# Kernel tuning notes

Hardware: AMD Instinct MI355X
Metric: run time of the kernel (lower is better)

## Reference

```python
import jax, jax.numpy as jnp
import numpy as np

# module hyperparams (from init_kwargs)
C, O, G, E, W, KS = 64, 64, 16, 128, 7, 2
AH, AS = 2, 2              # activate_height, activate_stride
D = C // G                 # kernel depth per group = 4
N = O // G                 # filters per group = 4
EPS = 1e-5                 # BatchNorm eps
LEAKY = 0.01               # LeakyReLU negative slope
B, T = 2, 512


def setup_inputs() -> dict:
    key = jax.random.key(0)
    k1, k2 = jax.random.split(key)
    x = jax.random.normal(k1, (B, C, E, T), dtype=jnp.float32)
    weight = jax.random.normal(k2, (O, D, E, W), dtype=jnp.float32) * 0.05
    gamma = jnp.ones((O,), jnp.float32)
    beta = jnp.zeros((O,), jnp.float32)
    return {"x": x, "weight": weight, "gamma": gamma, "beta": beta}


def reference(x, weight, gamma, beta):
    b, c, f, T_in = x.shape
    pad = W // 2
    xp = jnp.pad(x, ((0, 0), (0, 0), (0, 0), (pad, pad)))
    t = (T_in + 2 * pad - W) // KS + 1
    # unfold: window index grid [t, W]
    idx = KS * jnp.arange(t)[:, None] + jnp.arange(W)[None, :]
    xu = xp[..., idx]                        # [b, c, f, t, W]
    xu = xu.reshape(b, G, D, f, t, W)        # channel = (g d), group-major
    wg = weight.reshape(G, N, D, f, W)       # out = (g n)
    # broadcast elementwise mul -> [b, g, n, d, f, t, w]
    y = xu[:, :, None] * wg[None, :, :, :, :, None, :]
    y = y.reshape(b, O, D, f, t, W)          # (g n) -> o
    # BatchNorm3d over channel O, training-mode batch stats (biased var)
    mean = y.mean(axis=(0, 2, 3, 4, 5), keepdims=True)
    var = y.var(axis=(0, 2, 3, 4, 5), keepdims=True)
    y = (y - mean) * jax.lax.rsqrt(var + EPS)
    bshape = (1, O, 1, 1, 1, 1)
    y = y * gamma.reshape(bshape) + beta.reshape(bshape)
    ys = y.sum(axis=(2, 5))                  # [b, o, f, t]
    yp = jax.lax.reduce_window(ys, jnp.float32(0), jax.lax.add,
                               (1, 1, AH, 1), (1, 1, AS, 1), 'VALID')  # [b,o,fo,t]
    return jnp.where(yp >= 0, yp, LEAKY * yp)
```

## Files before the change

kernel.cpp:

```cpp
#include <hip/hip_runtime.h>

constexpr int Cc = 64, Oc = 64, Gc = 16, Ec = 128, Wc = 7;
constexpr int Dc = 4, Nc = 4, Bc = 2, Tc = 512, TTc = 256, FOc = 64;
constexpr float EPSf = 1e-5f, LEAKYf = 0.01f;
constexpr float Minv = 1.0f / 1835008.0f;


__global__ __launch_bounds__(256) void fused_k(const float* __restrict__ x,
                                               const float* __restrict__ wgt,
                                               float* __restrict__ raw,
                                               float* __restrict__ partials) {
  int bid = blockIdx.x;
  int fo  = bid & 63;
  int g   = (bid >> 6) & 15;
  int b   = bid >> 10;
  int tid = threadIdx.x;

  __shared__ float xs[8 * 520];
  __shared__ float wsm[224];
  __shared__ float rowsum[4][4][2];
  __shared__ float QL[8][7];

  int f2 = tid >> 7;
  int j  = tid & 127;
  float se2p[4], so2p[4];
#pragma unroll
  for (int dd = 0; dd < 4; ++dd) {
    const float4* src = (const float4*)(
        x + ((size_t)((b * Cc + g * Dc + dd) * Ec + 2 * fo + f2)) * Tc);
    float4 v = src[j];
    float* row = &xs[(dd * 2 + f2) * 520];
    int q0 = 4 + 4 * j;
    row[((q0 + 0) & 7) * 65 + ((q0 + 0) >> 3)] = v.x;
    row[((q0 + 1) & 7) * 65 + ((q0 + 1) >> 3)] = v.y;
    row[((q0 + 2) & 7) * 65 + ((q0 + 2) >> 3)] = v.z;
    row[((q0 + 3) & 7) * 65 + ((q0 + 3) >> 3)] = v.w;
    se2p[dd] = v.x * v.x + v.z * v.z;
    so2p[dd] = v.y * v.y + v.w * v.w;
  }
  if (tid < 64) {
    int r = tid >> 3, jj = tid & 7;
    int q = (jj < 4) ? jj : (512 + jj);
    xs[r * 520 + (q & 7) * 65 + (q >> 3)] = 0.f;
  }
  if (tid < 224) {
    int n = tid / 56, rr = tid % 56;
    int dd = rr / 14, r2 = rr % 14;
    int ff = r2 / 7, w = r2 % 7;
    int o = g * Nc + n;
    wsm[tid] = wgt[((size_t)((o * Dc + dd) * Ec + 2 * fo + ff)) * Wc + w];
  }
#pragma unroll
  for (int off = 1; off < 64; off <<= 1) {
#pragma unroll
    for (int dd = 0; dd < 4; ++dd) {
      se2p[dd] += __shfl_xor(se2p[dd], off);
      so2p[dd] += __shfl_xor(so2p[dd], off);
    }
  }
  int lane = tid & 63, wv = tid >> 6;
  if (lane == 0) {
#pragma unroll
    for (int dd = 0; dd < 4; ++dd) {
      rowsum[wv][dd][0] = se2p[dd];
      rowsum[wv][dd][1] = so2p[dd];
    }
  }
  __syncthreads();

  if (tid < 8) {
    int r = tid, ddi = r >> 1, f2i = r & 1;
    const float* row = &xs[r * 520];
    float e0 = row[260], e1 = row[325], e509 = row[129], e510 = row[194],
          e511 = row[259];
    float se2 = rowsum[f2i * 2][ddi][0] + rowsum[f2i * 2 + 1][ddi][0];
    float so2 = rowsum[f2i * 2][ddi][1] + rowsum[f2i * 2 + 1][ddi][1];
    QL[r][0] = so2 - e509 * e509 - e511 * e511;
    QL[r][1] = se2 - e510 * e510;
    QL[r][2] = so2 - e511 * e511;
    QL[r][3] = se2;
    QL[r][4] = so2;
    QL[r][5] = se2 - e0 * e0;
    QL[r][6] = so2 - e1 * e1;
  }
  __syncthreads();

  int n  = tid >> 6;
  int jj = tid & 63;
  float a0 = 0.f, a1 = 0.f, a2 = 0.f, a3 = 0.f;
#pragma unroll
  for (int r = 0; r < 8; ++r) {
    const float* row = &xs[r * 520];
    float xv[13];
#pragma unroll
    for (int i = 0; i < 13; ++i) {
      int c = 1 + i;
      xv[i] = row[(c & 7) * 65 + (c >> 3) + jj];
    }
    const float* wp = &wsm[(n * 8 + r) * 7];
#pragma unroll
    for (int w = 0; w < 7; ++w) {
      float wt = wp[w];
      a0 += xv[w]     * wt;
      a1 += xv[w + 2] * wt;
      a2 += xv[w + 4] * wt;
      a3 += xv[w + 6] * wt;
    }
  }
  int o = g * Nc + n;
  float4 res; res.x = a0; res.y = a1; res.z = a2; res.w = a3;
  *(float4*)(raw + ((size_t)((b * Oc + o) * FOc + fo)) * TTc + 4 * jj) = res;

  float msum = a0 + a1 + a2 + a3;
#pragma unroll
  for (int off = 1; off < 64; off <<= 1) msum += __shfl_xor(msum, off);
  if (jj == 0) partials[bid * 8 + n] = msum;

  if (tid < 4) {
    float vp = 0.f;
#pragma unroll
    for (int r = 0; r < 8; ++r) {
#pragma unroll
      for (int w = 0; w < 7; ++w) {
        float wt = wsm[(tid * 8 + r) * 7 + w];
        vp += QL[r][w] * wt * wt;
      }
    }
    partials[bid * 8 + 4 + tid] = vp;
  }
}

__global__ __launch_bounds__(256) void finish_k(const float* __restrict__ raw,
                                                const float* __restrict__ partials,
                                                const float* __restrict__ gamma,
                                                const float* __restrict__ beta,
                                                float* __restrict__ out) {
  int bid = blockIdx.x;
  int seg = bid & 15;
  int o   = (bid >> 4) & 63;
  int b   = bid >> 10;
  int tid = threadIdx.x;
  int g = o >> 2, n = o & 3;

  __shared__ float red[2][2];
  __shared__ float sAC[2];

  float mp = 0.f, vp = 0.f;
  if (tid < 128) {
    int b2 = tid >> 6, fo = tid & 63;
    const float* p = &partials[(size_t)(((b2 << 4) | g) << 6 | fo) * 8];
    mp = p[n];
    vp = p[4 + n];
  }
#pragma unroll
  for (int off = 1; off < 64; off <<= 1) {
    mp += __shfl_xor(mp, off);
    vp += __shfl_xor(vp, off);
  }
  int lane = tid & 63, wv = tid >> 6;
  if (lane == 0 && wv < 2) { red[wv][0] = mp; red[wv][1] = vp; }
  __syncthreads();
  if (tid == 0) {
    float mean = (red[0][0] + red[1][0]) * Minv;
    float e2   = (red[0][1] + red[1][1]) * Minv;
    float var  = e2 - mean * mean;
    float a    = gamma[o] * rsqrtf(var + EPSf);
    sAC[0] = a;
    sAC[1] = 56.0f * (beta[o] - a * mean);
  }
  __syncthreads();

  float a = sAC[0], c = sAC[1];
  size_t base = ((size_t)(b * Oc + o)) * (FOc * TTc) + seg * 1024 + tid * 4;
  float4 v = *(const float4*)(raw + base);
  float4 res;
  float r0 = a * v.x + c; res.x = (r0 >= 0.f) ? r0 : LEAKYf * r0;
  float r1 = a * v.y + c; res.y = (r1 >= 0.f) ? r1 : LEAKYf * r1;
  float r2 = a * v.z + c; res.z = (r2 >= 0.f) ? r2 : LEAKYf * r2;
  float r3 = a * v.w + c; res.w = (r3 >= 0.f) ? r3 : LEAKYf * r3;
  *(float4*)(out + base) = res;
}

extern "C" void kernel_launch(void* const* d_in, const int* in_sizes, int n_in,
                              void* d_out, int out_size, void* d_ws, size_t ws_size,
                              hipStream_t stream) {
  (void)in_sizes; (void)n_in; (void)out_size; (void)ws_size;
  const float* x     = (const float*)d_in[0];
  const float* w     = (const float*)d_in[1];
  const float* gamma = (const float*)d_in[2];
  const float* beta  = (const float*)d_in[3];
  float* raw      = (float*)d_ws;
  float* partials = raw + (size_t)Bc * Oc * FOc * TTc;
  fused_k<<<dim3(Bc * Gc * FOc), dim3(256), 0, stream>>>(x, w, raw, partials);
  finish_k<<<dim3(Bc * Oc * 16), dim3(256), 0, stream>>>(raw, partials, gamma,
                                                         beta, (float*)d_out);
}
```

Before: 92.87 us.

## Process two output rows per block with float4 shared layout and register tiling

The fused kernel now handles two pooled frequency rows per block, halving the grid. Input rows are staged in shared memory as padded float4 with a swizzled layout so both loads and window reads are vectorised. Each thread computes two output channels times four time steps, reusing the loaded x values across channels. Sum-of-squares statistics are recomputed from shared memory instead of during the load. This doubles shared memory per block and raises register pressure, which may lower occupancy.

Measured after the change: 91.48 us. No clear change (-1.5%).

```diff
diff --git a/kernel.cpp b/kernel.cpp
--- a/kernel.cpp
+++ b/kernel.cpp
@@ -5,128 +5,147 @@
 constexpr float EPSf = 1e-5f, LEAKYf = 0.01f;
 constexpr float Minv = 1.0f / 1835008.0f;
 
+
+__device__ __forceinline__ int FL4(int c) { return (c & 3) * 33 + (c >> 2); }
 
 __global__ __launch_bounds__(256) void fused_k(const float* __restrict__ x,
                                                const float* __restrict__ wgt,
                                                float* __restrict__ raw,
                                                float* __restrict__ partials) {
   int bid = blockIdx.x;
-  int fo  = bid & 63;
-  int g   = (bid >> 6) & 15;
-  int b   = bid >> 10;
-  int tid = threadIdx.x;
-
-  __shared__ float xs[8 * 520];
-  __shared__ float wsm[224];
-  __shared__ float rowsum[4][4][2];
-  __shared__ float QL[8][7];
-
-  int f2 = tid >> 7;
-  int j  = tid & 127;
-  float se2p[4], so2p[4];
-#pragma unroll
-  for (int dd = 0; dd < 4; ++dd) {
+  int fo2 = bid & 31;
+  int g   = (bid >> 5) & 15;
+  int b   = bid >> 9;
+  int t   = threadIdx.x;
+
+  __shared__ float xs[16 * 528];
+  __shared__ float wsm[512];
+  __shared__ float QS[16][2];
+  __shared__ float QL[16][7];
+
+  float4* xs4 = (float4*)xs;
+
+#pragma unroll
+  for (int k = 0; k < 8; ++k) {
+    int idx = t + 256 * k;
+    int lr = idx >> 7, jj = idx & 127;
+    int fo_l = lr >> 3, dd = (lr >> 1) & 3, f2 = lr & 1;
     const float4* src = (const float4*)(
-        x + ((size_t)((b * Cc + g * Dc + dd) * Ec + 2 * fo + f2)) * Tc);
-    float4 v = src[j];
-    float* row = &xs[(dd * 2 + f2) * 520];
-    int q0 = 4 + 4 * j;
-    row[((q0 + 0) & 7) * 65 + ((q0 + 0) >> 3)] = v.x;
-    row[((q0 + 1) & 7) * 65 + ((q0 + 1) >> 3)] = v.y;
-    row[((q0 + 2) & 7) * 65 + ((q0 + 2) >> 3)] = v.z;
-    row[((q0 + 3) & 7) * 65 + ((q0 + 3) >> 3)] = v.w;
-    se2p[dd] = v.x * v.x + v.z * v.z;
-    so2p[dd] = v.y * v.y + v.w * v.w;
-  }
-  if (tid < 64) {
-    int r = tid >> 3, jj = tid & 7;
-    int q = (jj < 4) ? jj : (512 + jj);
-    xs[r * 520 + (q & 7) * 65 + (q >> 3)] = 0.f;
-  }
-  if (tid < 224) {
-    int n = tid / 56, rr = tid % 56;
-    int dd = rr / 14, r2 = rr % 14;
-    int ff = r2 / 7, w = r2 % 7;
-    int o = g * Nc + n;
-    wsm[tid] = wgt[((size_t)((o * Dc + dd) * Ec + 2 * fo + ff)) * Wc + w];
-  }
-#pragma unroll
-  for (int off = 1; off < 64; off <<= 1) {
-#pragma unroll
-    for (int dd = 0; dd < 4; ++dd) {
-      se2p[dd] += __shfl_xor(se2p[dd], off);
-      so2p[dd] += __shfl_xor(so2p[dd], off);
-    }
-  }
-  int lane = tid & 63, wv = tid >> 6;
-  if (lane == 0) {
-#pragma unroll
-    for (int dd = 0; dd < 4; ++dd) {
-      rowsum[wv][dd][0] = se2p[dd];
-      rowsum[wv][dd][1] = so2p[dd];
-    }
-  }
-  __syncthreads();
-
-  if (tid < 8) {
-    int r = tid, ddi = r >> 1, f2i = r & 1;
-    const float* row = &xs[r * 520];
-    float e0 = row[260], e1 = row[325], e509 = row[129], e510 = row[194],
-          e511 = row[259];
-    float se2 = rowsum[f2i * 2][ddi][0] + rowsum[f2i * 2 + 1][ddi][0];
-    float so2 = rowsum[f2i * 2][ddi][1] + rowsum[f2i * 2 + 1][ddi][1];
-    QL[r][0] = so2 - e509 * e509 - e511 * e511;
-    QL[r][1] = se2 - e510 * e510;
-    QL[r][2] = so2 - e511 * e511;
-    QL[r][3] = se2;
-    QL[r][4] = so2;
-    QL[r][5] = se2 - e0 * e0;
-    QL[r][6] = so2 - e1 * e1;
-  }
-  __syncthreads();
-
-  int n  = tid >> 6;
-  int jj = tid & 63;
-  float a0 = 0.f, a1 = 0.f, a2 = 0.f, a3 = 0.f;
-#pragma unroll
-  for (int r = 0; r < 8; ++r) {
-    const float* row = &xs[r * 520];
-    float xv[13];
-#pragma unroll
-    for (int i = 0; i < 13; ++i) {
-      int c = 1 + i;
-      xv[i] = row[(c & 7) * 65 + (c >> 3) + jj];
-    }
-    const float* wp = &wsm[(n * 8 + r) * 7];
+        x + ((size_t)((b * Cc + g * Dc + dd) * Ec + 4 * fo2 + 2 * fo_l + f2)) * Tc);
+    float4 v = src[jj];
+    xs4[lr * 132 + FL4(jj + 1)] = v;
+  }
+  if (t < 32) {
+    int lr = t >> 1;
+    int c = (t & 1) ? 129 : 0;
+    xs4[lr * 132 + FL4(c)] = make_float4(0.f, 0.f, 0.f, 0.f);
+  }
+  if (t < 128) {
+#pragma unroll
+    for (int i = 0; i < 4; ++i) {
+      int s = t * 4 + i;
+      int w = s & 7, n = (s >> 3) & 3, lr8 = (s >> 5) & 7, fo_l = s >> 8;
+      int o = g * Nc + n, dd = lr8 >> 1, f = 4 * fo2 + 2 * fo_l + (lr8 & 1);
+      wsm[s] = (w < 7) ? wgt[((size_t)((o * Dc + dd) * Ec + f)) * Wc + w] : 0.f;
+    }
+  }
+  __syncthreads();
+
+  {
+    int row = t >> 4, sub = t & 15;
+    float se2 = 0.f, so2 = 0.f;
+#pragma unroll
+    for (int k = 0; k < 8; ++k) {
+      int c = 1 + sub + 16 * k;
+      float4 v = xs4[row * 132 + FL4(c)];
+      se2 += v.x * v.x + v.z * v.z;
+      so2 += v.y * v.y + v.w * v.w;
+    }
+#pragma unroll
+    for (int off = 1; off < 16; off <<= 1) {
+      se2 += __shfl_xor(se2, off);
+      so2 += __shfl_xor(so2, off);
+    }
+    if (sub == 0) { QS[row][0] = se2; QS[row][1] = so2; }
+  }
+
+  int wv = t >> 6, j = t & 63;
+  int fo_l = wv >> 1, n0 = (wv & 1) * 2;
+  int fo = fo2 * 2 + fo_l;
+  float acc0[4] = {0.f, 0.f, 0.f, 0.f}, acc1[4] = {0.f, 0.f, 0.f, 0.f};
+#pragma unroll
+  for (int lr8 = 0; lr8 < 8; ++lr8) {
+    const float4* rb = xs4 + (fo_l * 8 + lr8) * 132;
+    float4 X0 = rb[FL4(2 * j)];
+    float4 X1 = rb[FL4(2 * j + 1)];
+    float4 X2 = rb[FL4(2 * j + 2)];
+    float4 X3 = rb[FL4(2 * j + 3)];
+    float xq[16] = {X0.x, X0.y, X0.z, X0.w, X1.x, X1.y, X1.z, X1.w,
+                    X2.x, X2.y, X2.z, X2.w, X3.x, X3.y, X3.z, X3.w};
+    const float4* wb = (const float4*)&wsm[((fo_l * 8 + lr8) * 4 + n0) * 8];
+    float4 Wa0 = wb[0], Wa1 = wb[1], Wb0 = wb[2], Wb1 = wb[3];
+    float wA[7] = {Wa0.x, Wa0.y, Wa0.z, Wa0.w, Wa1.x, Wa1.y, Wa1.z};
+    float wB[7] = {Wb0.x, Wb0.y, Wb0.z, Wb0.w, Wb1.x, Wb1.y, Wb1.z};
 #pragma unroll
     for (int w = 0; w < 7; ++w) {
-      float wt = wp[w];
-      a0 += xv[w]     * wt;
-      a1 += xv[w + 2] * wt;
-      a2 += xv[w + 4] * wt;
-      a3 += xv[w + 6] * wt;
-    }
-  }
-  int o = g * Nc + n;
-  float4 res; res.x = a0; res.y = a1; res.z = a2; res.w = a3;
-  *(float4*)(raw + ((size_t)((b * Oc + o) * FOc + fo)) * TTc + 4 * jj) = res;
-
-  float msum = a0 + a1 + a2 + a3;
-#pragma unroll
-  for (int off = 1; off < 64; off <<= 1) msum += __shfl_xor(msum, off);
-  if (jj == 0) partials[bid * 8 + n] = msum;
-
-  if (tid < 4) {
+#pragma unroll
+      for (int s = 0; s < 4; ++s) {
+        float xv = xq[2 * s + w + 1];
+        acc0[s] += xv * wA[w];
+        acc1[s] += xv * wB[w];
+      }
+    }
+  }
+  {
+    int o0 = g * Nc + n0;
+    float4 r0 = make_float4(acc0[0], acc0[1], acc0[2], acc0[3]);
+    float4 r1 = make_float4(acc1[0], acc1[1], acc1[2], acc1[3]);
+    *(float4*)(raw + ((size_t)((b * Oc + o0) * FOc + fo)) * TTc + 4 * j) = r0;
+    *(float4*)(raw + ((size_t)((b * Oc + o0 + 1) * FOc + fo)) * TTc + 4 * j) = r1;
+  }
+  {
+    float ms0 = acc0[0] + acc0[1] + acc0[2] + acc0[3];
+    float ms1 = acc1[0] + acc1[1] + acc1[2] + acc1[3];
+#pragma unroll
+    for (int off = 1; off < 64; off <<= 1) {
+      ms0 += __shfl_xor(ms0, off);
+      ms1 += __shfl_xor(ms1, off);
+    }
+    if (j == 0) {
+      float* p = &partials[((size_t)((b * Gc + g) * FOc + fo)) * 8];
+      p[n0] = ms0;
+      p[n0 + 1] = ms1;
+    }
+  }
+  __syncthreads();
+
+  if (t < 16) {
+    int row = t;
+    const float* rowf = &xs[row * 528];
+    float e509 = rowf[129], e510 = rowf[130], e511 = rowf[131];
+    float e0 = rowf[132], e1 = rowf[133];
+    float se2 = QS[row][0], so2 = QS[row][1];
+    QL[row][0] = so2 - e509 * e509 - e511 * e511;
+    QL[row][1] = se2 - e510 * e510;
+    QL[row][2] = so2 - e511 * e511;
+    QL[row][3] = se2;
+    QL[row][4] = so2;
+    QL[row][5] = se2 - e0 * e0;
+    QL[row][6] = so2 - e1 * e1;
+  }
+  __syncthreads();
+  if (t < 8) {
+    int fl = t >> 2, n = t & 3;
     float vp = 0.f;
 #pragma unroll
-    for (int r = 0; r < 8; ++r) {
+    for (int lr8 = 0; lr8 < 8; ++lr8) {
 #pragma unroll
       for (int w = 0; w < 7; ++w) {
-        float wt = wsm[(tid * 8 + r) * 7 + w];
-        vp += QL[r][w] * wt * wt;
+        float wt = wsm[((fl * 8 + lr8) * 4 + n) * 8 + w];
+        vp += QL[fl * 8 + lr8][w] * wt * wt;
       }
     }
-    partials[bid * 8 + 4 + tid] = vp;
+    partials[((size_t)((b * Gc + g) * FOc + fo2 * 2 + fl)) * 8 + 4 + n] = vp;
   }
 }
 
@@ -191,7 +210,7 @@
   const float* beta  = (const float*)d_in[3];
   float* raw      = (float*)d_ws;
   float* partials = raw + (size_t)Bc * Oc * FOc * TTc;
-  fused_k<<<dim3(Bc * Gc * FOc), dim3(256), 0, stream>>>(x, w, raw, partials);
+  fused_k<<<dim3(Bc * Gc * 32), dim3(256), 0, stream>>>(x, w, raw, partials);
   finish_k<<<dim3(Bc * Oc * 16), dim3(256), 0, stream>>>(raw, partials, gamma,
                                                          beta, (float*)d_out);
 }
```
